# Performance work log

Hardware: AMD Instinct MI355X
Metric: run time of the kernel (lower is better)

Reference implementation:

```python
import jax, jax.numpy as jnp
import numpy as np

N_EMBED = 1024
CUTOFFS = [20000, 40000, 200000]
N_VOCAB = 267735
N_EMBEDS = [1024, 256, 64, 16]  # n_embed // 4**i
N_TOKENS = 1024
STARTS = [0] + CUTOFFS
ENDS = CUTOFFS + [N_VOCAB]


def setup_inputs() -> dict:
    key = jax.random.key(0)
    ks = jax.random.split(key, 16)
    s = 0.02
    inp = {}
    inp["hidden"] = jax.random.normal(ks[0], (N_TOKENS, N_EMBED), jnp.float32)
    inp["target"] = jax.random.randint(ks[1], (N_TOKENS,), 0, N_VOCAB)
    # head: layers[0] = Linear(1024, 20000); clusters = Linear(1024, 3)
    inp["W_head"] = jax.random.normal(ks[2], (ENDS[0], N_EMBEDS[0]), jnp.float32) * s
    inp["b_head"] = jax.random.normal(ks[3], (ENDS[0],), jnp.float32) * s
    inp["W_clusters"] = jax.random.normal(ks[4], (len(CUTOFFS), N_EMBED), jnp.float32) * s
    inp["b_clusters"] = jax.random.normal(ks[5], (len(CUTOFFS),), jnp.float32) * s
    # tails: projections[i-1] = Linear(1024, n_embeds[i], bias=False); layers[i] = Linear(n_embeds[i], end-start)
    k = 6
    for i in (1, 2, 3):
        d_i = N_EMBEDS[i]
        v_i = ENDS[i] - STARTS[i]
        inp[f"P{i}"] = jax.random.normal(ks[k], (d_i, N_EMBED), jnp.float32) * s
        inp[f"W{i}"] = jax.random.normal(ks[k + 1], (v_i, d_i), jnp.float32) * s
        inp[f"b{i}"] = jax.random.normal(ks[k + 2], (v_i,), jnp.float32) * s
        k += 3
    return inp


def reference(hidden, target, W_head, b_head, W_clusters, b_clusters,
              P1, W1, b1, P2, W2, b2, P3, W3, b3):
    # head logits: [N, cutoff0 + n_clusters]
    head_logit = jnp.concatenate(
        [hidden @ W_head.T + b_head, hidden @ W_clusters.T + b_clusters], axis=1)
    head_logprob = jax.nn.log_softmax(head_logit, axis=1)
    head_dim = head_logprob.shape[1]

    cuts = jnp.asarray(CUTOFFS)
    cluster_id = (target[:, None] >= cuts[None, :]).sum(axis=1)  # 0..3

    # cluster 0: direct head gather
    t0 = jnp.clip(target, 0, ENDS[0] - 1)
    lp0 = jnp.take_along_axis(head_logprob, t0[:, None], axis=1)[:, 0]

    def tail_lp(P, W, b, i):
        proj = hidden @ P.T                      # [N, d_i]
        tlp = jax.nn.log_softmax(proj @ W.T + b, axis=1)  # [N, v_i]
        ti = jnp.clip(target - STARTS[i], 0, W.shape[0] - 1)
        g = jnp.take_along_axis(tlp, ti[:, None], axis=1)[:, 0]
        # torch: head_logprob_i[:, -i]
        return head_logprob[:, head_dim - i] + g

    lp1 = tail_lp(P1, W1, b1, 1)
    lp2 = tail_lp(P2, W2, b2, 2)
    lp3 = tail_lp(P3, W3, b3, 3)

    logprob = jnp.select(
        [cluster_id == 0, cluster_id == 1, cluster_id == 2, cluster_id == 3],
        [lp0, lp1, lp2, lp3])
    return -logprob  # per-token NLL, keep_order ordering
```

## Files before the change

kernel.cpp:

```cpp
#include <hip/hip_runtime.h>
#include <cstdint>
#include <cstddef>

typedef __attribute__((ext_vector_type(8))) short short8;
typedef __attribute__((ext_vector_type(4))) float f32x4;

#define LOG2E 1.4426950408889634f
#define LN2   0.6931471805599453f

__device__ __forceinline__ unsigned short f2bf(float x) {
    unsigned u = __float_as_uint(x);
    u += 0x7FFFu + ((u >> 16) & 1u);
    return (unsigned short)(u >> 16);
}
__device__ __forceinline__ float bf2f(unsigned short h) {
    return __uint_as_float(((unsigned)h) << 16);
}

__device__ __forceinline__ void gload_lds16(const void* g, void* l) {
    __builtin_amdgcn_global_load_lds(
        (const __attribute__((address_space(1))) unsigned int*)g,
        (__attribute__((address_space(3))) unsigned int*)l, 16, 0, 0);
}

__device__ __forceinline__ float sum16(const f32x4 (&accv)[4][4], int ni,
                                       const float (&bvv)[4][4]) {
    float e[16];
#pragma unroll
    for (int q = 0; q < 16; ++q)
        e[q] = exp2f(fmaf(accv[q >> 2][ni][q & 3], LOG2E, bvv[q >> 2][q & 3]));
#pragma unroll
    for (int st = 1; st < 16; st <<= 1)
#pragma unroll
        for (int q = 0; q < 16; q += st * 2)
            e[q] += e[q + st];
    float sm = e[0];
    sm += __shfl_xor(sm, 16, 64);
    sm += __shfl_xor(sm, 32, 64);
    return sm;
}

__global__ void mega_convert(const float* __restrict__ hidden,
                             const float* __restrict__ P1, const float* __restrict__ P2,
                             const float* __restrict__ P3,
                             const float* __restrict__ W_head, const float* __restrict__ W_clu,
                             const float* __restrict__ W1,
                             unsigned short* __restrict__ hbf, unsigned short* __restrict__ Pb,
                             unsigned short* __restrict__ Whb, unsigned short* __restrict__ W1b,
                             int nWh, int nClu, int nZp, int nW1) {
    long i = (long)blockIdx.x * 256 + threadIdx.x;
    const float* src;
    unsigned short* dst;
    if (i < nWh)                      { src = W_head; dst = Whb; }
    else if ((i -= nWh) < nClu)       { src = W_clu;  dst = Whb + (size_t)20000 * 1024; }
    else if ((i -= nClu) < nZp) {
        *(unsigned long long*)(Whb + (size_t)20003 * 1024 + i * 4) = 0ull;
        return;
    }
    else if ((i -= nZp) < nW1)        { src = W1;     dst = W1b; }
    else if ((i -= nW1) < 262144)     { src = hidden; dst = hbf; }
    else if ((i -= 262144) < 65536)   { src = P1;     dst = Pb; }
    else if ((i -= 65536) < 16384)    { src = P2;     dst = Pb + (size_t)256 * 1024; }
    else if ((i -= 16384) < 4096)     { src = P3;     dst = Pb + (size_t)320 * 1024; }
    else if ((i -= 4096) < 12288) {
        *(unsigned long long*)(Pb + (size_t)336 * 1024 + i * 4) = 0ull;
        return;
    } else return;
    float4 v = *(const float4*)(src + (size_t)i * 4);
    unsigned long long p = (unsigned long long)f2bf(v.x)
                         | ((unsigned long long)f2bf(v.y) << 16)
                         | ((unsigned long long)f2bf(v.z) << 32)
                         | ((unsigned long long)f2bf(v.w) << 48);
    *(unsigned long long*)(dst + (size_t)i * 4) = p;
}

__global__ __launch_bounds__(1024)
void compact_tokens(const int* __restrict__ target, int* __restrict__ cnt,
                    int* __restrict__ slotc) {
    const int t = threadIdx.x;
    const int tgt = target[t];
    const int cid = (tgt >= 20000) + (tgt >= 40000) + (tgt >= 200000);
    const int wave = t >> 6, lane = t & 63;
    unsigned long long lt = (lane == 0) ? 0ull : (~0ull >> (64 - lane));
    __shared__ int wtot[3][16];
    __shared__ int wbase[3][16];
    unsigned long long bal[3];
#pragma unroll
    for (int c = 1; c <= 3; ++c) {
        unsigned long long b = __ballot(cid == c);
        if (lane == 0) wtot[c - 1][wave] = (int)__popcll(b);
        bal[c - 1] = b;
    }
    __syncthreads();
    if (t < 3) {
        int s = 0;
        for (int w = 0; w < 16; ++w) { wbase[t][w] = s; s += wtot[t][w]; }
        cnt[t + 1] = s;
        if (t == 0) cnt[0] = 1024;
    }
    __syncthreads();
    int sl = t;
    if (cid > 0) sl = wbase[cid - 1][wave] + (int)__popcll(bal[cid - 1] & lt);
    slotc[t] = sl | (cid << 16);
}

__global__ __launch_bounds__(256)
void proj_mfma(const unsigned short* __restrict__ Hb,
               const unsigned short* __restrict__ Pb,
               const int* __restrict__ slotc,
               unsigned short* __restrict__ Hc1,
               unsigned short* __restrict__ Hc2,
               unsigned short* __restrict__ Hc3) {
    __shared__ __align__(16) char As[16384];
    __shared__ __align__(16) char Bs[16384];
    __shared__ int sl_s[128];
    const int tid  = threadIdx.x;
    const int lane = tid & 63;
    const int wid  = tid >> 6;
    const int wm = wid >> 1, wn = wid & 1;
    const int tt = blockIdx.x, dt = blockIdx.y;
    const int t0 = tt * 128, d0 = dt * 128;

    f32x4 acc[4][4];
    const f32x4 zero = {0.f, 0.f, 0.f, 0.f};
#pragma unroll
    for (int i = 0; i < 4; ++i)
#pragma unroll
        for (int j = 0; j < 4; ++j) acc[i][j] = zero;

    for (int kt = 0; kt < 16; ++kt) {
#pragma unroll
        for (int j = 0; j < 4; ++j) {
            int lds_off = wid * 4096 + j * 1024;
            int o = lds_off + lane * 16;
            int r = o >> 7;
            int b = (o & 127) ^ ((r & 7) << 4);
            gload_lds16(Hb + (size_t)(t0 + r) * 1024 + kt * 64 + (b >> 1), As + lds_off);
        }
#pragma unroll
        for (int j = 0; j < 4; ++j) {
            int lds_off = wid * 4096 + j * 1024;
            int o = lds_off + lane * 16;
            int r = o >> 7;
            int b = (o & 127) ^ ((r & 7) << 4);
            gload_lds16(Pb + (size_t)(d0 + r) * 1024 + kt * 64 + (b >> 1), Bs + lds_off);
        }
        __syncthreads();
#pragma unroll
        for (int kk = 0; kk < 2; ++kk) {
            const int kbyte = (kk * 32 + ((lane >> 4) << 3)) * 2;
            short8 a[4], b[4];
#pragma unroll
            for (int mi = 0; mi < 4; ++mi) {
                int row = wm * 64 + mi * 16 + (lane & 15);
                int off = (row * 128 + kbyte) ^ ((row & 7) << 4);
                a[mi] = *(const short8*)(As + off);
            }
#pragma unroll
            for (int ni = 0; ni < 4; ++ni) {
                int row = wn * 64 + ni * 16 + (lane & 15);
                int off = (row * 128 + kbyte) ^ ((row & 7) << 4);
                b[ni] = *(const short8*)(Bs + off);
            }
#pragma unroll
            for (int mi = 0; mi < 4; ++mi)
#pragma unroll
                for (int ni = 0; ni < 4; ++ni)
                    acc[mi][ni] = __builtin_amdgcn_mfma_f32_16x16x32_bf16(a[mi], b[ni], acc[mi][ni], 0, 0, 0);
        }
        __syncthreads();
    }

    if (tid < 128) sl_s[tid] = slotc[t0 + tid];
    __syncthreads();

#pragma unroll
    for (int ni = 0; ni < 4; ++ni) {
        int dg = d0 + wn * 64 + ni * 16 + (lane & 15);
        unsigned short* base;
        int c_d, dd, stride;
        if (dg < 256)      { c_d = 1; dd = dg;       base = Hc1; stride = 256; }
        else if (dg < 320) { c_d = 2; dd = dg - 256; base = Hc2; stride = 64;  }
        else               { c_d = 3; dd = dg - 320; base = Hc3; stride = 64;  }
#pragma unroll
        for (int mi = 0; mi < 4; ++mi)
#pragma unroll
            for (int r = 0; r < 4; ++r) {
                int tl = wm * 64 + mi * 16 + ((lane >> 4) << 2) + r;
                int sc = sl_s[tl];
                if ((sc >> 16) == c_d)
                    base[(size_t)(sc & 0xFFFF) * stride + dd] = f2bf(acc[mi][ni][r]);
            }
    }
}

template<bool BF16B>
__device__ __forceinline__ void gemm_lse_dev(
        char* Ws, char* Hs, float* bias_s, float* red,
        const unsigned short* __restrict__ Wb,
        const float* __restrict__ Wfa, const float* __restrict__ Wfb,
        int NsplitW, int NsplitB, int N, int K, int Kv, int KTILES,
        const float* __restrict__ bias1, const float* __restrict__ bias2,
        const unsigned short* __restrict__ H, int t0, int n0,
        float* __restrict__ pS_out) {
    const int tid  = threadIdx.x;
    const int lane = tid & 63;
    const int wid  = tid >> 6;
    const int wm = wid >> 1, wn = wid & 1;
    const bool clean = BF16B && (n0 + 128 <= NsplitW);

    if (tid < 128) {
        int v = n0 + tid;
        bias_s[tid] = (v < NsplitB) ? bias1[v] * LOG2E
                    : (v < N)       ? bias2[v - NsplitB] * LOG2E
                                    : -INFINITY;
    }

    f32x4 acc[4][4];
    const f32x4 zero = {0.f, 0.f, 0.f, 0.f};
#pragma unroll
    for (int i = 0; i < 4; ++i)
#pragma unroll
        for (int j = 0; j < 4; ++j) acc[i][j] = zero;

    for (int kt = 0; kt < KTILES; ++kt) {
        if (clean) {
#pragma unroll
            for (int j = 0; j < 4; ++j) {
                int lds_off = wid * 4096 + j * 1024;
                int o = lds_off + lane * 16;
                int r = o >> 7;
                int b = (o & 127) ^ ((r & 7) << 4);
                gload_lds16(Wb + (size_t)(n0 + r) * K + kt * 64 + (b >> 1), Ws + lds_off);
            }
        } else {
#pragma unroll
            for (int it = 0; it < 4; ++it) {
                int c = tid + it * 256;
                int row = c >> 3, kc = (c & 7) << 3;
                int v = n0 + row;
                int kg = kt * 64 + kc;
                unsigned short hh[8] = {0,0,0,0,0,0,0,0};
                if (v < NsplitB) {
                    if (BF16B) {
                        *(int4*)hh = *(const int4*)(Wb + (size_t)v * K + kg);
                    } else if (kg + 8 <= Kv) {
                        const float* p = Wfa + (size_t)v * Kv;
                        float4 u0 = *(const float4*)(p + kg);
                        float4 u1 = *(const float4*)(p + kg + 4);
                        hh[0]=f2bf(u0.x); hh[1]=f2bf(u0.y); hh[2]=f2bf(u0.z); hh[3]=f2bf(u0.w);
                        hh[4]=f2bf(u1.x); hh[5]=f2bf(u1.y); hh[6]=f2bf(u1.z); hh[7]=f2bf(u1.w);
                    }
                } else if (v < N && Wfb != nullptr) {
                    const float* p = Wfb + (size_t)(v - NsplitB) * K;
                    float4 u0 = *(const float4*)(p + kg);
                    float4 u1 = *(const float4*)(p + kg + 4);
                    hh[0]=f2bf(u0.x); hh[1]=f2bf(u0.y); hh[2]=f2bf(u0.z); hh[3]=f2bf(u0.w);
                    hh[4]=f2bf(u1.x); hh[5]=f2bf(u1.y); hh[6]=f2bf(u1.z); hh[7]=f2bf(u1.w);
                }
                int off = (row * 128 + kc * 2) ^ ((row & 7) << 4);
                *(int4*)(Ws + off) = *(const int4*)hh;
            }
        }
#pragma unroll
        for (int j = 0; j < 4; ++j) {
            int lds_off = wid * 4096 + j * 1024;
            int o = lds_off + lane * 16;
            int r = o >> 7;
            int b = (o & 127) ^ ((r & 7) << 4);
            gload_lds16(H + (size_t)(t0 + r) * K + kt * 64 + (b >> 1), Hs + lds_off);
        }
        __syncthreads();
#pragma unroll
        for (int kk = 0; kk < 2; ++kk) {
            const int kbyte = (kk * 32 + ((lane >> 4) << 3)) * 2;
            short8 a[4], b[4];
#pragma unroll
            for (int mi = 0; mi < 4; ++mi) {
                int row = wm * 64 + mi * 16 + (lane & 15);
                int off = (row * 128 + kbyte) ^ ((row & 7) << 4);
                a[mi] = *(const short8*)(Ws + off);
            }
#pragma unroll
            for (int ni = 0; ni < 4; ++ni) {
                int row = wn * 64 + ni * 16 + (lane & 15);
                int off = (row * 128 + kbyte) ^ ((row & 7) << 4);
                b[ni] = *(const short8*)(Hs + off);
            }
#pragma unroll
            for (int mi = 0; mi < 4; ++mi)
#pragma unroll
                for (int ni = 0; ni < 4; ++ni)
                    acc[mi][ni] = __builtin_amdgcn_mfma_f32_16x16x32_bf16(a[mi], b[ni], acc[mi][ni], 0, 0, 0);
        }
        __syncthreads();
    }

    float bvv[4][4];
#pragma unroll
    for (int mi = 0; mi < 4; ++mi)
#pragma unroll
        for (int r = 0; r < 4; ++r)
            bvv[mi][r] = bias_s[wm * 64 + mi * 16 + ((lane >> 4) << 2) + r];

#pragma unroll
    for (int ni = 0; ni < 4; ++ni) {
        float sm = sum16(acc, ni, bvv);
        if ((lane >> 4) == 0)
            red[wm * 128 + wn * 64 + ni * 16 + lane] = sm;
    }
    __syncthreads();
    if (tid < 128)
        pS_out[t0 + tid] = red[tid] + red[128 + tid];
}

template<int KV>
__device__ __forceinline__ void tail_res_dev(
        char* Ws, char* Hs, float* bias_s, float* red,
        const float* __restrict__ Wf, int N,
        const float* __restrict__ bias,
        const unsigned short* __restrict__ Hc, int cntc, int n0,
        float* __restrict__ pS_out) {
    const int tid = threadIdx.x, lane = tid & 63, wid = tid >> 6;
    const int wm = wid >> 1, wn = wid & 1;

#pragma unroll
    for (int it = 0; it < 4; ++it) {
        int c = tid + it * 256;
        int row = c >> 3, kc = (c & 7) << 3;
        int v = n0 + row;
        unsigned short hh[8] = {0,0,0,0,0,0,0,0};
        if (v < N && kc < KV) {
            const float* p = Wf + (size_t)v * KV + kc;
            float4 u0 = *(const float4*)p;
            float4 u1 = *(const float4*)(p + 4);
            hh[0]=f2bf(u0.x); hh[1]=f2bf(u0.y); hh[2]=f2bf(u0.z); hh[3]=f2bf(u0.w);
            hh[4]=f2bf(u1.x); hh[5]=f2bf(u1.y); hh[6]=f2bf(u1.z); hh[7]=f2bf(u1.w);
        }
        int off = (row * 128 + kc * 2) ^ ((row & 7) << 4);
        *(int4*)(Ws + off) = *(const int4*)hh;
    }
    if (tid < 128) {
        int v = n0 + tid;
        bias_s[tid] = (v < N) ? bias[v] * LOG2E : -INFINITY;
    }
    __syncthreads();
    short8 a[2][4];
#pragma unroll
    for (int kk = 0; kk < 2; ++kk)
#pragma unroll
        for (int mi = 0; mi < 4; ++mi) {
            int row = wm * 64 + mi * 16 + (lane & 15);
            int kbyte = (kk * 32 + ((lane >> 4) << 3)) * 2;
            a[kk][mi] = *(const short8*)(Ws + ((row * 128 + kbyte) ^ ((row & 7) << 4)));
        }
    float bvv[4][4];
#pragma unroll
    for (int mi = 0; mi < 4; ++mi)
#pragma unroll
        for (int r = 0; r < 4; ++r)
            bvv[mi][r] = bias_s[wm * 64 + mi * 16 + ((lane >> 4) << 2) + r];
    const int ntt = (cntc + 127) >> 7;

    for (int tt = 0; tt < ntt; ++tt) {
#pragma unroll
        for (int j = 0; j < 4; ++j) {
            int lds_off = wid * 4096 + j * 1024;
            int o = lds_off + lane * 16;
            int r = o >> 7;
            int b = (o & 127) ^ ((r & 7) << 4);
            gload_lds16(Hc + (size_t)(tt * 128 + r) * 64 + (b >> 1), Hs + lds_off);
        }
        __syncthreads();
        f32x4 acc[4][4];
        const f32x4 zero = {0.f, 0.f, 0.f, 0.f};
#pragma unroll
        for (int i = 0; i < 4; ++i)
#pragma unroll
            for (int j = 0; j < 4; ++j) acc[i][j] = zero;
#pragma unroll
        for (int kk = 0; kk < 2; ++kk) {
            const int kbyte = (kk * 32 + ((lane >> 4) << 3)) * 2;
            short8 b[4];
#pragma unroll
            for (int ni = 0; ni < 4; ++ni) {
                int row = wn * 64 + ni * 16 + (lane & 15);
                b[ni] = *(const short8*)(Hs + ((row * 128 + kbyte) ^ ((row & 7) << 4)));
            }
#pragma unroll
            for (int mi = 0; mi < 4; ++mi)
#pragma unroll
                for (int ni = 0; ni < 4; ++ni)
                    acc[mi][ni] = __builtin_amdgcn_mfma_f32_16x16x32_bf16(a[kk][mi], b[ni], acc[mi][ni], 0, 0, 0);
        }
        const int cur = tt & 1;
        float* redc = red + cur * 256;
#pragma unroll
        for (int ni = 0; ni < 4; ++ni) {
            float sm = sum16(acc, ni, bvv);
            if ((lane >> 4) == 0)
                redc[wm * 128 + wn * 64 + ni * 16 + lane] = sm;
        }
        __syncthreads();
        if (tid < 128)
            pS_out[tt * 128 + tid] = redc[tid] + redc[128 + tid];
    }
}

#define NB_H 1280
#define NB_2 1250
#define NB_3 530
#define NB_1 1256
template<bool PRE>
__global__ __launch_bounds__(256)
void fused_lse(const unsigned short* __restrict__ Whb,
               const float* __restrict__ W_head, const float* __restrict__ W_clu,
               const unsigned short* __restrict__ W1b, const float* __restrict__ W1,
               const float* __restrict__ W2, const float* __restrict__ W3,
               const float* __restrict__ b_head, const float* __restrict__ b_clu,
               const float* __restrict__ b1, const float* __restrict__ b2,
               const float* __restrict__ b3,
               const unsigned short* __restrict__ hbf,
               const unsigned short* __restrict__ Hc1,
               const unsigned short* __restrict__ Hc2,
               const unsigned short* __restrict__ Hc3,
               const int* __restrict__ cnt,
               float* __restrict__ pSh, float* __restrict__ pS1,
               float* __restrict__ pS2, float* __restrict__ pS3) {
    __shared__ __align__(16) char smem[37376];
    char* Ws = smem;
    char* Hs = smem + 16384;
    float* bias_s = (float*)(smem + 32768);
    float* red    = (float*)(smem + 33280);
    const int b = blockIdx.x;

    if (b < NB_H) {
        const int x = b & 7, i = b >> 3;
        const int nt = x * 20 + (i >> 3);
        const int tt = i & 7;
        if (nt >= 157) return;
        if (PRE)
            gemm_lse_dev<true>(Ws, Hs, bias_s, red,
                               Whb, nullptr, nullptr,
                               20096, 20000, 20003, 1024, 1024, 16,
                               b_head, b_clu, hbf, tt * 128, nt * 128,
                               pSh + (size_t)nt * 1024);
        else
            gemm_lse_dev<false>(Ws, Hs, bias_s, red,
                                nullptr, W_head, W_clu,
                                20000, 20000, 20003, 1024, 1024, 16,
                                b_head, b_clu, hbf, tt * 128, nt * 128,
                                pSh + (size_t)nt * 1024);
    } else if (b < NB_H + NB_2) {
        const int v = b - NB_H;
        tail_res_dev<64>(Ws, Hs, bias_s, red, W2, 160000, b2,
                         Hc2, cnt[2], v * 128, pS2 + (size_t)v * 1024);
    } else if (b < NB_H + NB_2 + NB_3) {
        const int v = b - NB_H - NB_2;
        tail_res_dev<16>(Ws, Hs, bias_s, red, W3, 67735, b3,
                         Hc3, cnt[3], v * 128, pS3 + (size_t)v * 1024);
    } else {
        const int local = b - NB_H - NB_2 - NB_3;
        const int tt = local & 7, nt = local >> 3;
        if (tt * 128 >= cnt[1]) return;
        if (PRE)
            gemm_lse_dev<true>(Ws, Hs, bias_s, red,
                               W1b, nullptr, nullptr,
                               20000, 20000, 20000, 256, 256, 4,
                               b1, nullptr, Hc1, tt * 128, nt * 128,
                               pS1 + (size_t)nt * 1024);
        else
            gemm_lse_dev<false>(Ws, Hs, bias_s, red,
                                nullptr, W1, nullptr,
                                20000, 20000, 20000, 256, 256, 4,
                                b1, nullptr, Hc1, tt * 128, nt * 128,
                                pS1 + (size_t)nt * 1024);
    }
}

__global__ __launch_bounds__(256)
void reduce_part(const float* __restrict__ pSh, int nth,
                 const float* __restrict__ pS1, int nt1,
                 const float* __restrict__ pS2, int nt2,
                 const float* __restrict__ pS3, int nt3,
                 float* __restrict__ pRs) {
    const int c = blockIdx.y, z = blockIdx.z;
    const float* PS = (c == 0) ? pSh : (c == 1) ? pS1 : (c == 2) ? pS2 : pS3;
    const int nt = (c == 0) ? nth : (c == 1) ? nt1 : (c == 2) ? nt2 : nt3;
    const int lane = threadIdx.x & 63;
    const int seg  = threadIdx.x >> 6;
    const int t = blockIdx.x * 64 + lane;
    float s = 0.f;
    for (int i = z * 4 + seg; i < nt; i += 64)
        s += PS[(size_t)i * 1024 + t];
    __shared__ float rs[4][64];
    rs[seg][lane] = s;
    __syncthreads();
    if (seg == 0) {
        s += rs[1][lane] + rs[2][lane] + rs[3][lane];
        pRs[((size_t)c * 16 + z) * 1024 + t] = s;
    }
}

__global__ __launch_bounds__(256)
void reduce_final(const float* __restrict__ pRs, float* __restrict__ lse) {
    const int c = blockIdx.y;
    const int lane = threadIdx.x & 63;
    const int seg  = threadIdx.x >> 6;
    const int t = blockIdx.x * 64 + lane;
    float s = 0.f;
#pragma unroll
    for (int z = 0; z < 4; ++z)
        s += pRs[((size_t)c * 16 + seg * 4 + z) * 1024 + t];
    __shared__ float rs[4][64];
    rs[seg][lane] = s;
    __syncthreads();
    if (seg == 0) {
        s += rs[1][lane] + rs[2][lane] + rs[3][lane];
        lse[c * 1024 + t] = LN2 * log2f(s);
    }
}

__global__ void finalize(const float* __restrict__ hidden, const int* __restrict__ target,
                         const float* __restrict__ W_head, const float* __restrict__ b_head,
                         const float* __restrict__ W_clu, const float* __restrict__ b_clu,
                         const float* __restrict__ W1, const float* __restrict__ b1,
                         const float* __restrict__ W2, const float* __restrict__ b2,
                         const float* __restrict__ W3, const float* __restrict__ b3,
                         const unsigned short* __restrict__ Hc1,
                         const unsigned short* __restrict__ Hc2,
                         const unsigned short* __restrict__ Hc3,
                         const int* __restrict__ slotc,
                         const float* __restrict__ lse,
                         float* __restrict__ out) {
    const int t = blockIdx.x;
    const int lane = threadIdx.x;
    const int tgt = target[t];
    const int cid = (tgt >= 20000) + (tgt >= 40000) + (tgt >= 200000);
    const int j = (cid == 0) ? tgt : (20003 - cid);
    const float* wr = (j < 20000) ? (W_head + (size_t)j * 1024)
                                  : (W_clu + (size_t)(j - 20000) * 1024);
    float acc = 0.f;
#pragma unroll
    for (int i = 0; i < 4; ++i) {
        int k4 = lane + i * 64;
        float4 h = *(const float4*)(hidden + (size_t)t * 1024 + k4 * 4);
        float4 w = *(const float4*)(wr + k4 * 4);
        acc += h.x * w.x + h.y * w.y + h.z * w.z + h.w * w.w;
    }
#pragma unroll
    for (int msk = 1; msk < 64; msk <<= 1) acc += __shfl_xor(acc, msk, 64);
    float bj = (j < 20000) ? b_head[j] : b_clu[j - 20000];
    float res = (acc + bj) - lse[t];
    if (cid > 0) {
        const int starts[4] = {0, 20000, 40000, 200000};
        const int dims[4]   = {0, 256, 64, 16};
        const int slot = slotc[t] & 0xFFFF;
        const float* Wt = (cid == 1) ? W1 : (cid == 2) ? W2 : W3;
        const float* bt = (cid == 1) ? b1 : (cid == 2) ? b2 : b3;
        const unsigned short* pr = (cid == 1) ? Hc1 + (size_t)slot * 256
                                 : (cid == 2) ? Hc2 + (size_t)slot * 64
                                              : Hc3 + (size_t)slot * 64;
        int ti = tgt - starts[cid];
        int d  = dims[cid];
        const float* wt = Wt + (size_t)ti * d;
        float a2 = 0.f;
        for (int k = lane; k < d; k += 64) a2 += bf2f(pr[k]) * wt[k];
#pragma unroll
        for (int msk = 1; msk < 64; msk <<= 1) a2 += __shfl_xor(a2, msk, 64);
        res += (a2 + bt[ti]) - lse[cid * 1024 + slot];
    }
    if (lane == 0) out[t] = -res;
}

extern "C" void kernel_launch(void* const* d_in, const int* in_sizes, int n_in,
                              void* d_out, int out_size, void* d_ws, size_t ws_size,
                              hipStream_t stream) {
    const float* hidden = (const float*)d_in[0];
    const int*   target = (const int*)d_in[1];
    const float* W_head = (const float*)d_in[2];
    const float* b_head = (const float*)d_in[3];
    const float* W_clu  = (const float*)d_in[4];
    const float* b_clu  = (const float*)d_in[5];
    const float* P1 = (const float*)d_in[6];
    const float* W1 = (const float*)d_in[7];
    const float* b1 = (const float*)d_in[8];
    const float* P2 = (const float*)d_in[9];
    const float* W2 = (const float*)d_in[10];
    const float* b2 = (const float*)d_in[11];
    const float* P3 = (const float*)d_in[12];
    const float* W3 = (const float*)d_in[13];
    const float* b3 = (const float*)d_in[14];
    float* out = (float*)d_out;

    char* ws = (char*)d_ws;
    size_t off = 0;
    auto alloc = [&](size_t bytes) -> char* {
        char* p = ws + off;
        off += (bytes + 255) & ~(size_t)255;
        return p;
    };
    const int NT_H = 157;
    const int NT_1 = 157;
    const int NT_2 = 1250;
    const int NT_3 = 530;

    unsigned short* hbf   = (unsigned short*)alloc((size_t)1024 * 1024 * 2);
    unsigned short* Pb    = (unsigned short*)alloc((size_t)384 * 1024 * 2);
    int* cnt   = (int*)alloc(4 * 4);
    int* slotc = (int*)alloc(1024 * 4);
    unsigned short* Hc1 = (unsigned short*)alloc((size_t)1024 * 256 * 2);
    unsigned short* Hc2 = (unsigned short*)alloc((size_t)1024 * 64 * 2);
    unsigned short* Hc3 = (unsigned short*)alloc((size_t)1024 * 64 * 2);
    float* pSh = (float*)alloc((size_t)1024 * NT_H * 4);
    float* pS1 = (float*)alloc((size_t)1024 * NT_1 * 4);
    float* pS2 = (float*)alloc((size_t)1024 * NT_2 * 4);
    float* pS3 = (float*)alloc((size_t)1024 * NT_3 * 4);
    float* lse = (float*)alloc((size_t)4 * 1024 * 4);
    float* pRs = (float*)alloc((size_t)4 * 16 * 1024 * 4);
    unsigned short* Whb = (unsigned short*)alloc((size_t)20096 * 1024 * 2);
    unsigned short* W1b = (unsigned short*)alloc((size_t)20000 * 256 * 2);
    const bool pre = (off <= ws_size);

    const int nWh  = pre ? 5120000 : 0;
    const int nClu = pre ? 768 : 0;
    const int nZp  = pre ? 23808 : 0;
    const int nW1  = pre ? 1280000 : 0;
    const long nChunks = (long)nWh + nClu + nZp + nW1 + 360448;
    mega_convert<<<(unsigned)((nChunks + 255) / 256), 256, 0, stream>>>(
        hidden, P1, P2, P3, W_head, W_clu, W1, hbf, Pb, Whb, W1b,
        nWh, nClu, nZp, nW1);
    compact_tokens<<<1, 1024, 0, stream>>>(target, cnt, slotc);
    proj_mfma<<<dim3(8, 3), 256, 0, stream>>>(hbf, Pb, slotc, Hc1, Hc2, Hc3);

    const int NB_TOT = NB_H + NB_2 + NB_3 + NB_1;
    if (pre)
        fused_lse<true><<<NB_TOT, 256, 0, stream>>>(
            Whb, W_head, W_clu, W1b, W1, W2, W3,
            b_head, b_clu, b1, b2, b3,
            hbf, Hc1, Hc2, Hc3, cnt, pSh, pS1, pS2, pS3);
    else
        fused_lse<false><<<NB_TOT, 256, 0, stream>>>(
            Whb, W_head, W_clu, W1b, W1, W2, W3,
            b_head, b_clu, b1, b2, b3,
            hbf, Hc1, Hc2, Hc3, cnt, pSh, pS1, pS2, pS3);

    reduce_part<<<dim3(16, 4, 16), 256, 0, stream>>>(pSh, NT_H, pS1, NT_1,
                                                     pS2, NT_2, pS3, NT_3, pRs);
    reduce_final<<<dim3(16, 4), 256, 0, stream>>>(pRs, lse);

    finalize<<<1024, 64, 0, stream>>>(hidden, target,
                                      W_head, b_head, W_clu, b_clu,
                                      W1, b1, W2, b2, W3, b3,
                                      Hc1, Hc2, Hc3, slotc, lse, out);
}
```

Baseline: 180.6 us.

## Interleave fused_lse work types across blocks and drop W1 bf16 conversion

Reorders the block-to-work mapping in fused_lse so that head GEMM tiles and cluster-2 tail tiles alternate in a 5-slot pattern per group of 8 blocks, with cluster-3 tiles and cluster-1 tiles placed after them. This mixes compute-heavy and memory-heavy blocks instead of running them in contiguous phases. The cluster-1 GEMM now reads the fp32 W1 directly, with one block per vocab tile looping over all of that cluster's token tiles, so the bf16 conversion of W1 and its buffer are removed. The price is fp32 loads of W1 inside the GEMM and a serial loop over token tiles in each cluster-1 block, which may create long-running stragglers.

```diff
diff --git a/kernel.cpp b/kernel.cpp
--- a/kernel.cpp
+++ b/kernel.cpp
@@ -44,10 +44,9 @@
                              const float* __restrict__ P1, const float* __restrict__ P2,
                              const float* __restrict__ P3,
                              const float* __restrict__ W_head, const float* __restrict__ W_clu,
-                             const float* __restrict__ W1,
                              unsigned short* __restrict__ hbf, unsigned short* __restrict__ Pb,
-                             unsigned short* __restrict__ Whb, unsigned short* __restrict__ W1b,
-                             int nWh, int nClu, int nZp, int nW1) {
+                             unsigned short* __restrict__ Whb,
+                             int nWh, int nClu, int nZp) {
     long i = (long)blockIdx.x * 256 + threadIdx.x;
     const float* src;
     unsigned short* dst;
@@ -57,8 +56,7 @@
         *(unsigned long long*)(Whb + (size_t)20003 * 1024 + i * 4) = 0ull;
         return;
     }
-    else if ((i -= nZp) < nW1)        { src = W1;     dst = W1b; }
-    else if ((i -= nW1) < 262144)     { src = hidden; dst = hbf; }
+    else if ((i -= nZp) < 262144)     { src = hidden; dst = hbf; }
     else if ((i -= 262144) < 65536)   { src = P1;     dst = Pb; }
     else if ((i -= 65536) < 16384)    { src = P2;     dst = Pb + (size_t)256 * 1024; }
     else if ((i -= 16384) < 4096)     { src = P3;     dst = Pb + (size_t)320 * 1024; }
@@ -407,15 +405,12 @@
     }
 }
 
-#define NB_H 1280
-#define NB_2 1250
-#define NB_3 530
-#define NB_1 1256
+#define NSLOT 435
 template<bool PRE>
 __global__ __launch_bounds__(256)
 void fused_lse(const unsigned short* __restrict__ Whb,
                const float* __restrict__ W_head, const float* __restrict__ W_clu,
-               const unsigned short* __restrict__ W1b, const float* __restrict__ W1,
+               const float* __restrict__ W1,
                const float* __restrict__ W2, const float* __restrict__ W3,
                const float* __restrict__ b_head, const float* __restrict__ b_clu,
                const float* __restrict__ b1, const float* __restrict__ b2,
@@ -433,11 +428,15 @@
     float* bias_s = (float*)(smem + 32768);
     float* red    = (float*)(smem + 33280);
     const int b = blockIdx.x;
-
-    if (b < NB_H) {
-        const int x = b & 7, i = b >> 3;
-        const int nt = x * 20 + (i >> 3);
-        const int tt = i & 7;
+    const int x = b & 7;
+    const int i = b >> 3;
+    const int m = i % 5, j = i / 5;
+
+    if (m == 0 || m == 2) {
+        const int h = 2 * j + (m >> 1);
+        if (h >= 160) return;
+        const int nt = x * 20 + (h >> 3);
+        const int tt = h & 7;
         if (nt >= 157) return;
         if (PRE)
             gemm_lse_dev<true>(Ws, Hs, bias_s, red,
@@ -451,30 +450,28 @@
                                 20000, 20000, 20003, 1024, 1024, 16,
                                 b_head, b_clu, hbf, tt * 128, nt * 128,
                                 pSh + (size_t)nt * 1024);
-    } else if (b < NB_H + NB_2) {
-        const int v = b - NB_H;
+    } else if (m == 1 || m == 3) {
+        const int v = (2 * j + ((m - 1) >> 1)) * 8 + x;
+        if (v >= 1250) return;
         tail_res_dev<64>(Ws, Hs, bias_s, red, W2, 160000, b2,
                          Hc2, cnt[2], v * 128, pS2 + (size_t)v * 1024);
-    } else if (b < NB_H + NB_2 + NB_3) {
-        const int v = b - NB_H - NB_2;
-        tail_res_dev<16>(Ws, Hs, bias_s, red, W3, 67735, b3,
-                         Hc3, cnt[3], v * 128, pS3 + (size_t)v * 1024);
     } else {
-        const int local = b - NB_H - NB_2 - NB_3;
-        const int tt = local & 7, nt = local >> 3;
-        if (tt * 128 >= cnt[1]) return;
-        if (PRE)
-            gemm_lse_dev<true>(Ws, Hs, bias_s, red,
-                               W1b, nullptr, nullptr,
-                               20000, 20000, 20000, 256, 256, 4,
-                               b1, nullptr, Hc1, tt * 128, nt * 128,
-                               pS1 + (size_t)nt * 1024);
-        else
-            gemm_lse_dev<false>(Ws, Hs, bias_s, red,
-                                nullptr, W1, nullptr,
-                                20000, 20000, 20000, 256, 256, 4,
-                                b1, nullptr, Hc1, tt * 128, nt * 128,
-                                pS1 + (size_t)nt * 1024);
+        if (j < 67) {
+            const int v = j * 8 + x;
+            if (v >= 530) return;
+            tail_res_dev<16>(Ws, Hs, bias_s, red, W3, 67735, b3,
+                             Hc3, cnt[3], v * 128, pS3 + (size_t)v * 1024);
+        } else {
+            const int nt = (j - 67) * 8 + x;
+            if (nt >= 157) return;
+            const int c1 = cnt[1];
+            for (int t0 = 0; t0 < c1; t0 += 128)
+                gemm_lse_dev<false>(Ws, Hs, bias_s, red,
+                                    nullptr, W1, nullptr,
+                                    20000, 20000, 20000, 256, 256, 4,
+                                    b1, nullptr, Hc1, t0, nt * 128,
+                                    pS1 + (size_t)nt * 1024);
+        }
     }
 }
 
@@ -619,29 +616,26 @@
     float* lse = (float*)alloc((size_t)4 * 1024 * 4);
     float* pRs = (float*)alloc((size_t)4 * 16 * 1024 * 4);
     unsigned short* Whb = (unsigned short*)alloc((size_t)20096 * 1024 * 2);
-    unsigned short* W1b = (unsigned short*)alloc((size_t)20000 * 256 * 2);
     const bool pre = (off <= ws_size);
 
     const int nWh  = pre ? 5120000 : 0;
     const int nClu = pre ? 768 : 0;
     const int nZp  = pre ? 23808 : 0;
-    const int nW1  = pre ? 1280000 : 0;
-    const long nChunks = (long)nWh + nClu + nZp + nW1 + 360448;
+    const long nChunks = (long)nWh + nClu + nZp + 360448;
     mega_convert<<<(unsigned)((nChunks + 255) / 256), 256, 0, stream>>>(
-        hidden, P1, P2, P3, W_head, W_clu, W1, hbf, Pb, Whb, W1b,
-        nWh, nClu, nZp, nW1);
+        hidden, P1, P2, P3, W_head, W_clu, hbf, Pb, Whb, nWh, nClu, nZp);
     compact_tokens<<<1, 1024, 0, stream>>>(target, cnt, slotc);
     proj_mfma<<<dim3(8, 3), 256, 0, stream>>>(hbf, Pb, slotc, Hc1, Hc2, Hc3);
 
-    const int NB_TOT = NB_H + NB_2 + NB_3 + NB_1;
+    const int NB_TOT = 8 * NSLOT;
     if (pre)
         fused_lse<true><<<NB_TOT, 256, 0, stream>>>(
-            Whb, W_head, W_clu, W1b, W1, W2, W3,
+            Whb, W_head, W_clu, W1, W2, W3,
             b_head, b_clu, b1, b2, b3,
             hbf, Hc1, Hc2, Hc3, cnt, pSh, pS1, pS2, pS3);
     else
         fused_lse<false><<<NB_TOT, 256, 0, stream>>>(
-            Whb, W_head, W_clu, W1b, W1, W2, W3,
+            Whb, W_head, W_clu, W1, W2, W3,
             b_head, b_clu, b1, b2, b3,
             hbf, Hc1, Hc2, Hc3, cnt, pSh, pS1, pS2, pS3);
 
```

Result: faster. 170.7 us (-5.5%).
